# Performance work log

Measured on AMD Instinct MI355X. Metric: run time of the kernel, lower is better.

The kernel has to match this reference:

```python
import jax, jax.numpy as jnp
import numpy as np

B = 16384          # batch_size
NF = 50            # n_fields
K = 16             # embedding_dim
V = 1_000_000      # input_dim (vocab)
H = 400            # fc hidden
NNZ = B * NF


def _xavier(key, shape):
    fan_in, fan_out = shape
    lim = (6.0 / (fan_in + fan_out)) ** 0.5
    return jax.random.uniform(key, shape, minval=-lim, maxval=lim, dtype=jnp.float32)


def setup_inputs() -> dict:
    key = jax.random.key(0)
    ks = jax.random.split(key, 12)
    feats = jax.random.randint(ks[0], (NNZ,), 0, V)
    # n_fields contiguous features per sample (required by view(batch_size,-1))
    index = jnp.repeat(jnp.arange(B), NF)
    values = jax.random.uniform(ks[1], (NNZ,), dtype=jnp.float32)
    bias = jnp.zeros((1, 1), jnp.float32)
    weights = _xavier(ks[2], (V, 1))
    embedding = _xavier(ks[3], (V, K))
    d = NF * K  # 800
    W0 = _xavier(ks[4], (d, H))
    b0 = jax.random.normal(ks[5], (1, 1), jnp.float32)
    W1 = _xavier(ks[6], (H, H))
    b1 = jax.random.normal(ks[7], (1, 1), jnp.float32)
    W2 = _xavier(ks[8], (H, 1))
    b2 = jax.random.normal(ks[9], (1, 1), jnp.float32)
    return dict(index=index, feats=feats, values=values, bias=bias,
                weights=weights, embedding=embedding,
                W0=W0, b0=b0, W1=W1, b1=b1, W2=W2, b2=b2, batch_size=B)


def reference(index, feats, values, bias, weights, embedding,
              W0, b0, W1, b1, W2, b2, batch_size):
    # gather (F.embedding)
    w = weights[feats, 0]              # [nnz]
    emb = embedding[feats]             # [nnz, K]

    # first order: segment-sum of w*v, plus bias ([B] + [1,1] -> [1,B], as in torch)
    first = jax.ops.segment_sum(w * values, index, num_segments=batch_size) + bias

    # second order: FM pooling trick, fused over all K dims in one segment reduce
    ev = emb * values[:, None]                                        # [nnz, K]
    s1 = jax.ops.segment_sum(ev, index, num_segments=batch_size)      # [B, K]
    s2 = jax.ops.segment_sum(ev * ev, index, num_segments=batch_size) # [B, K]
    second = 0.5 * jnp.sum(s1 * s1 - s2, axis=1)                      # [B]

    # higher order MLP (relu on every layer, scalar biases)
    x = emb.reshape(batch_size, -1)    # [B, NF*K]
    x = jax.nn.relu(x @ W0 + b0)
    x = jax.nn.relu(x @ W1 + b1)
    x = jax.nn.relu(x @ W2 + b2)       # [B, 1]
    higher = x.reshape(-1)             # [B]

    return jax.nn.sigmoid(first + second + higher)  # [1, B]
```

## Files before the change

### kernel.cpp

```cpp
#include <hip/hip_runtime.h>
#include <hip/hip_bf16.h>


#define BATCH 16384
#define NFLD  50
#define EK    16
#define DDIM  800
#define HDIM  400
#define HPAD  416
#define NPAD  512

#define TB_W0 400
#define TB_W1 208
#define TBLK  (TB_W0 + TB_W1)
#define GBLK  (BATCH / 16)

#define MROWS 64
#define NCOLS 448
#define WCOLS 112
#define NFRAG 7
#define P1    (DDIM / 32)
#define P2    (HPAD / 32)
#define H0S   424
#define NCHUNK (NCOLS / 16)

typedef __attribute__((ext_vector_type(8))) __bf16 bf16x8;
typedef __attribute__((ext_vector_type(4))) float  f32x4;

typedef const __attribute__((address_space(1))) unsigned int* gas_u32p;
typedef __attribute__((address_space(3))) unsigned int*       las_u32p;

__device__ __forceinline__ void gld_lds16(const void* g, void* l) {
    __builtin_amdgcn_global_load_lds((gas_u32p)g, (las_u32p)l, 16, 0, 0);
}

__device__ __forceinline__ bf16x8 cvt8(const float4 a, const float4 b) {
    union { __hip_bfloat16 h[8]; bf16x8 v; } u;
    u.h[0] = __float2bfloat16(a.x); u.h[1] = __float2bfloat16(a.y);
    u.h[2] = __float2bfloat16(a.z); u.h[3] = __float2bfloat16(a.w);
    u.h[4] = __float2bfloat16(b.x); u.h[5] = __float2bfloat16(b.y);
    u.h[6] = __float2bfloat16(b.z); u.h[7] = __float2bfloat16(b.w);
    return u.v;
}

__global__ __launch_bounds__(256) void prep_kernel(
    const float* __restrict__ W0, const float* __restrict__ W1,
    __hip_bfloat16* __restrict__ W0t, __hip_bfloat16* __restrict__ W1t,
    const int* __restrict__ feats, const float* __restrict__ values,
    const float* __restrict__ biasp, const float* __restrict__ weights,
    const float* __restrict__ embedding, float* __restrict__ fs)
{
    const int bid = blockIdx.x;
    if (bid < TBLK) {
        const int which = bid >= TB_W0;
        const int i  = which ? bid - TB_W0 : bid;
        const int nx = which ? 13 : 25;
        const int bx = i % nx, by = i / nx;
        const float* src = which ? W1 : W0;
        __hip_bfloat16* dst = which ? W1t : W0t;
        const int srcK = which ? HDIM : DDIM;
        const int dstCols = which ? HPAD : DDIM;

        __shared__ float tile[32][33];
        const int tx = threadIdx.x & 31, ty = threadIdx.x >> 5;
        const int k0 = bx * 32, n0 = by * 32;
#pragma unroll
        for (int r = 0; r < 4; ++r) {
            int k = k0 + ty + r * 8;
            int n = n0 + tx;
            float v = (k < srcK && n < HDIM) ? src[(long)k * HDIM + n] : 0.f;
            tile[ty + r * 8][tx] = v;
        }
        __syncthreads();
#pragma unroll
        for (int r = 0; r < 4; ++r) {
            int n = n0 + ty + r * 8;
            int k = k0 + tx;
            if (k < dstCols)
                dst[(long)n * dstCols + k] = __float2bfloat16(tile[tx][ty + r * 8]);
        }
        return;
    }

    const int wave = threadIdx.x >> 6;
    const int lane = threadIdx.x & 63;
    const int r    = lane >> 2, c = lane & 3;
    const int sbase = (bid - TBLK) * 16 + wave * 4;

    int   f[4] = {0, 0, 0, 0};
    float v[4] = {0.f, 0.f, 0.f, 0.f};
    float wsum[4] = {0.f, 0.f, 0.f, 0.f};
#pragma unroll
    for (int q = 0; q < 4; ++q) {
        const long base = (long)(sbase + q) * NFLD;
        if (lane < NFLD) {
            f[q] = feats[base + lane];
            v[q] = values[base + lane];
            wsum[q] = weights[f[q]] * v[q];
        }
    }

    int   fj[4][4]; float vj[4][4];
#pragma unroll
    for (int q = 0; q < 4; ++q)
#pragma unroll
        for (int p = 0; p < 4; ++p) {
            const int j = p * 16 + r;
            if (p < 3 || r < 2) {
                fj[q][p] = __shfl(f[q], j);
                vj[q][p] = __shfl(v[q], j);
            }
        }
    float4 e[4][4];
#pragma unroll
    for (int q = 0; q < 4; ++q)
#pragma unroll
        for (int p = 0; p < 4; ++p)
            if (p < 3 || r < 2)
                e[q][p] = *(const float4*)(embedding + (long)fj[q][p] * EK + c * 4);

#pragma unroll
    for (int q = 0; q < 4; ++q) {
        const int s = sbase + q;
        f32x4 s1 = {0.f, 0.f, 0.f, 0.f}, s2 = {0.f, 0.f, 0.f, 0.f};
#pragma unroll
        for (int p = 0; p < 4; ++p) {
            const int j = p * 16 + r;
            if (p < 3 || r < 2) {
                f32x4 ef = {e[q][p].x, e[q][p].y, e[q][p].z, e[q][p].w};
                f32x4 ev = ef * vj[q][p];
                s1 += ev;
                s2 += ev * ev;
            }
        }
#pragma unroll
        for (int m = 4; m <= 32; m <<= 1) {
            s1.x += __shfl_xor(s1.x, m); s1.y += __shfl_xor(s1.y, m);
            s1.z += __shfl_xor(s1.z, m); s1.w += __shfl_xor(s1.w, m);
            s2.x += __shfl_xor(s2.x, m); s2.y += __shfl_xor(s2.y, m);
            s2.z += __shfl_xor(s2.z, m); s2.w += __shfl_xor(s2.w, m);
        }
        float t = (s1.x * s1.x - s2.x) + (s1.y * s1.y - s2.y)
                + (s1.z * s1.z - s2.z) + (s1.w * s1.w - s2.w);
        t += __shfl_xor(t, 1); t += __shfl_xor(t, 2);
        float w = wsum[q];
        w += __shfl_xor(w, 1);  w += __shfl_xor(w, 2);
        w += __shfl_xor(w, 4);  w += __shfl_xor(w, 8);
        w += __shfl_xor(w, 16); w += __shfl_xor(w, 32);
        if (lane == 0) fs[s] = w + 0.5f * t + biasp[0];
    }
}

__global__ __launch_bounds__(512, 2) void fused_mlp_kernel(
    const int* __restrict__ feats, const float* __restrict__ embedding,
    const __hip_bfloat16* __restrict__ W0t, const __hip_bfloat16* __restrict__ W1t,
    const float* __restrict__ b0p, const float* __restrict__ b1p,
    const float* __restrict__ W2, const float* __restrict__ b2p,
    const float* __restrict__ fs, float* __restrict__ out)
{
    __shared__ __align__(16) __hip_bfloat16 sB[2][NCOLS * 32];
    __shared__ __align__(16) __hip_bfloat16 h0p[MROWS * H0S];
    __shared__ int   sfeat[MROWS * NFLD];
    __shared__ float red[MROWS][4];

    const int tid  = threadIdx.x;
    const int wave = tid >> 6, lane = tid & 63;
    const int l16  = lane & 15, quad = lane >> 4;
    const int waveM = wave & 1, waveN = wave >> 1;
    const int m0 = blockIdx.x * MROWS;

    for (int i = tid; i < MROWS * NFLD; i += 512)
        sfeat[i] = feats[(long)m0 * NFLD + i];

    const float b0 = b0p[0];
    const float b1 = b1p[0];

    auto stageB = [&](const __hip_bfloat16* Bt, int ldb, int k0, int h) {
#pragma unroll
        for (int c = 0; c < 4; ++c) {
            const int ch = wave + c * 8;
            if (ch < NCHUNK) {
                const __hip_bfloat16* src =
                    Bt + (long)(ch * 16 + (lane >> 2)) * ldb + k0 + (lane & 3) * 8;
                gld_lds16(src, &sB[h][ch * 512 + lane * 8]);
            }
        }
    };

    auto loadA = [&](int p, float4* rg) {
        const int f  = p * 2 + (quad >> 1);
        const int d0 = (quad & 1) * 8;
#pragma unroll
        for (int i = 0; i < 2; ++i) {
            const int row = waveM * 32 + i * 16 + l16;
            const long fi = sfeat[row * NFLD + f];
            const float* ep = embedding + fi * EK + d0;
            rg[2 * i]     = *(const float4*)ep;
            rg[2 * i + 1] = *(const float4*)(ep + 4);
        }
    };

    f32x4 acc[2][NFRAG] = {};

    __syncthreads();
    float4 ra[4];
    loadA(0, ra);
    stageB(W0t, DDIM, 0, 0);
    __syncthreads();

#pragma unroll
    for (int p = 0; p < P1; ++p) {
        const int h = p & 1;
        float4 rn[4];
        if (p + 1 < P1) {
            stageB(W0t, DDIM, (p + 1) * 32, h ^ 1);
            loadA(p + 1, rn);
        }
        bf16x8 af[2];
        af[0] = cvt8(ra[0], ra[1]);
        af[1] = cvt8(ra[2], ra[3]);
        bf16x8 bfr[NFRAG];
#pragma unroll
        for (int j = 0; j < NFRAG; ++j)
            bfr[j] = *(const bf16x8*)&sB[h][(waveN * WCOLS + j * 16 + l16) * 32 + quad * 8];
#pragma unroll
        for (int i = 0; i < 2; ++i)
#pragma unroll
            for (int j = 0; j < NFRAG; ++j)
                acc[i][j] = __builtin_amdgcn_mfma_f32_16x16x32_bf16(
                    af[i], bfr[j], acc[i][j], 0, 0, 0);
        __syncthreads();
        if (p + 1 < P1) {
#pragma unroll
            for (int q = 0; q < 4; ++q) ra[q] = rn[q];
        }
    }

#pragma unroll
    for (int i = 0; i < 2; ++i)
#pragma unroll
        for (int j = 0; j < NFRAG; ++j) {
            const int col = waveN * WCOLS + j * 16 + l16;
            if (col < HPAD) {
#pragma unroll
                for (int r = 0; r < 4; ++r) {
                    const int row = waveM * 32 + i * 16 + quad * 4 + r;
                    float v = acc[i][j][r] + b0;
                    v = v > 0.f ? v : 0.f;
                    if (col >= HDIM) v = 0.f;
                    h0p[row * H0S + col] = __float2bfloat16(v);
                }
            }
        }

    f32x4 acc2[2][NFRAG] = {};
    stageB(W1t, HPAD, 0, 0);
    float w2v[NFRAG];
#pragma unroll
    for (int j = 0; j < NFRAG; ++j) {
        const int col = waveN * WCOLS + j * 16 + l16;
        w2v[j] = (col < HDIM) ? W2[col] : 0.f;
    }
    __syncthreads();

#pragma unroll
    for (int p = 0; p < P2; ++p) {
        const int h = p & 1;
        if (p + 1 < P2)
            stageB(W1t, HPAD, (p + 1) * 32, h ^ 1);
        bf16x8 af[2];
#pragma unroll
        for (int i = 0; i < 2; ++i)
            af[i] = *(const bf16x8*)&h0p[(waveM * 32 + i * 16 + l16) * H0S + p * 32 + quad * 8];
        bf16x8 bfr[NFRAG];
#pragma unroll
        for (int j = 0; j < NFRAG; ++j)
            bfr[j] = *(const bf16x8*)&sB[h][(waveN * WCOLS + j * 16 + l16) * 32 + quad * 8];
#pragma unroll
        for (int i = 0; i < 2; ++i)
#pragma unroll
            for (int j = 0; j < NFRAG; ++j)
                acc2[i][j] = __builtin_amdgcn_mfma_f32_16x16x32_bf16(
                    af[i], bfr[j], acc2[i][j], 0, 0, 0);
        __syncthreads();
    }

#pragma unroll
    for (int i = 0; i < 2; ++i)
#pragma unroll
        for (int r = 0; r < 4; ++r) {
            float ps = 0.f;
#pragma unroll
            for (int j = 0; j < NFRAG; ++j) {
                float v = acc2[i][j][r] + b1;
                v = v > 0.f ? v : 0.f;
                ps += v * w2v[j];
            }
            ps += __shfl_xor(ps, 1); ps += __shfl_xor(ps, 2);
            ps += __shfl_xor(ps, 4); ps += __shfl_xor(ps, 8);
            if (l16 == 0)
                red[waveM * 32 + i * 16 + quad * 4 + r][waveN] = ps;
        }
    __syncthreads();

    if (tid < MROWS) {
        const float s = (red[tid][0] + red[tid][1]) + (red[tid][2] + red[tid][3]);
        float hv = s + b2p[0];
        hv = hv > 0.f ? hv : 0.f;
        const float z = fs[m0 + tid] + hv;
        out[m0 + tid] = 1.f / (1.f + __expf(-z));
    }
}

extern "C" void kernel_launch(void* const* d_in, const int* in_sizes, int n_in,
                              void* d_out, int out_size, void* d_ws, size_t ws_size,
                              hipStream_t stream)
{
    const int*   feats     = (const int*)d_in[1];
    const float* values    = (const float*)d_in[2];
    const float* bias      = (const float*)d_in[3];
    const float* weights   = (const float*)d_in[4];
    const float* embedding = (const float*)d_in[5];
    const float* W0 = (const float*)d_in[6];
    const float* b0 = (const float*)d_in[7];
    const float* W1 = (const float*)d_in[8];
    const float* b1 = (const float*)d_in[9];
    const float* W2 = (const float*)d_in[10];
    const float* b2 = (const float*)d_in[11];

    char* ws = (char*)d_ws;
    size_t off = 0;
    auto alloc = [&](size_t bytes) {
        void* p = ws + off;
        off += (bytes + 255) & ~(size_t)255;
        return p;
    };
    float*          fs   = (float*)alloc((size_t)BATCH * 4);
    __hip_bfloat16* W0t  = (__hip_bfloat16*)alloc((size_t)NPAD * DDIM * 2);
    __hip_bfloat16* W1t  = (__hip_bfloat16*)alloc((size_t)NPAD * HPAD * 2);
    (void)ws_size; (void)in_sizes; (void)n_in; (void)out_size;

    prep_kernel<<<dim3(TBLK + GBLK), 256, 0, stream>>>(
        W0, W1, W0t, W1t, feats, values, bias, weights, embedding, fs);
    fused_mlp_kernel<<<dim3(BATCH / MROWS), 512, 0, stream>>>(
        feats, embedding, W0t, W1t, b0, b1, W2, b2, fs, (float*)d_out);
}
```

Before: 187.1 us.

## Materialize bf16 embedding matrix in prep kernel and stage A tiles via LDS DMA

The prep kernel, which already gathers the embeddings for the FM terms, now also writes them as a bf16 [B,800] matrix in workspace. The MLP kernel then loads A tiles with global_load_lds DMA alongside the W0 tiles, instead of doing a dependent feature lookup, float gather and register-side bf16 conversion per step. The K loops are also restructured to stage two k-tiles and then compute both between barriers, rather than using a prefetch-next pipeline. This removes the scattered gather latency from the GEMM loop, at the cost of writing and re-reading about 26 MB of intermediate data and losing compute/load overlap inside the loop.

```diff
diff --git a/kernel.cpp b/kernel.cpp
--- a/kernel.cpp
+++ b/kernel.cpp
@@ -34,21 +34,13 @@
     __builtin_amdgcn_global_load_lds((gas_u32p)g, (las_u32p)l, 16, 0, 0);
 }
 
-__device__ __forceinline__ bf16x8 cvt8(const float4 a, const float4 b) {
-    union { __hip_bfloat16 h[8]; bf16x8 v; } u;
-    u.h[0] = __float2bfloat16(a.x); u.h[1] = __float2bfloat16(a.y);
-    u.h[2] = __float2bfloat16(a.z); u.h[3] = __float2bfloat16(a.w);
-    u.h[4] = __float2bfloat16(b.x); u.h[5] = __float2bfloat16(b.y);
-    u.h[6] = __float2bfloat16(b.z); u.h[7] = __float2bfloat16(b.w);
-    return u.v;
-}
-
 __global__ __launch_bounds__(256) void prep_kernel(
     const float* __restrict__ W0, const float* __restrict__ W1,
     __hip_bfloat16* __restrict__ W0t, __hip_bfloat16* __restrict__ W1t,
     const int* __restrict__ feats, const float* __restrict__ values,
     const float* __restrict__ biasp, const float* __restrict__ weights,
-    const float* __restrict__ embedding, float* __restrict__ fs)
+    const float* __restrict__ embedding,
+    float* __restrict__ fs, __hip_bfloat16* __restrict__ x)
 {
     const int bid = blockIdx.x;
     if (bid < TBLK) {
@@ -131,6 +123,10 @@
                 f32x4 ev = ef * vj[q][p];
                 s1 += ev;
                 s2 += ev * ev;
+                __hip_bfloat16 pk[4] = {
+                    __float2bfloat16(e[q][p].x), __float2bfloat16(e[q][p].y),
+                    __float2bfloat16(e[q][p].z), __float2bfloat16(e[q][p].w)};
+                *(uint2*)&x[(long)s * DDIM + j * EK + c * 4] = *(uint2*)pk;
             }
         }
 #pragma unroll
@@ -152,15 +148,15 @@
 }
 
 __global__ __launch_bounds__(512, 2) void fused_mlp_kernel(
-    const int* __restrict__ feats, const float* __restrict__ embedding,
+    const __hip_bfloat16* __restrict__ x,
     const __hip_bfloat16* __restrict__ W0t, const __hip_bfloat16* __restrict__ W1t,
     const float* __restrict__ b0p, const float* __restrict__ b1p,
     const float* __restrict__ W2, const float* __restrict__ b2p,
     const float* __restrict__ fs, float* __restrict__ out)
 {
+    __shared__ __align__(16) __hip_bfloat16 sA[2][MROWS * 32];
     __shared__ __align__(16) __hip_bfloat16 sB[2][NCOLS * 32];
     __shared__ __align__(16) __hip_bfloat16 h0p[MROWS * H0S];
-    __shared__ int   sfeat[MROWS * NFLD];
     __shared__ float red[MROWS][4];
 
     const int tid  = threadIdx.x;
@@ -168,58 +164,44 @@
     const int l16  = lane & 15, quad = lane >> 4;
     const int waveM = wave & 1, waveN = wave >> 1;
     const int m0 = blockIdx.x * MROWS;
-
-    for (int i = tid; i < MROWS * NFLD; i += 512)
-        sfeat[i] = feats[(long)m0 * NFLD + i];
+    const int rlane = lane >> 2, clane = (lane & 3) * 8;
 
     const float b0 = b0p[0];
     const float b1 = b1p[0];
 
-    auto stageB = [&](const __hip_bfloat16* Bt, int ldb, int k0, int h) {
+    auto stage1 = [&](int p, int h) {
+        const int k0 = p * 32;
+#pragma unroll
+        for (int c = 0; c < 4; ++c) {
+            const int idx = wave * 4 + c;
+            if (idx < 4) {
+                gld_lds16(x + (long)(m0 + idx * 16 + rlane) * DDIM + k0 + clane,
+                          &sA[h][idx * 512 + lane * 8]);
+            } else {
+                const int ch = idx - 4;
+                gld_lds16(W0t + (long)(ch * 16 + rlane) * DDIM + k0 + clane,
+                          &sB[h][ch * 512 + lane * 8]);
+            }
+        }
+    };
+    auto stage2 = [&](int p, int h) {
+        const int k0 = p * 32;
 #pragma unroll
         for (int c = 0; c < 4; ++c) {
             const int ch = wave + c * 8;
             if (ch < NCHUNK) {
-                const __hip_bfloat16* src =
-                    Bt + (long)(ch * 16 + (lane >> 2)) * ldb + k0 + (lane & 3) * 8;
-                gld_lds16(src, &sB[h][ch * 512 + lane * 8]);
-            }
-        }
-    };
-
-    auto loadA = [&](int p, float4* rg) {
-        const int f  = p * 2 + (quad >> 1);
-        const int d0 = (quad & 1) * 8;
-#pragma unroll
-        for (int i = 0; i < 2; ++i) {
-            const int row = waveM * 32 + i * 16 + l16;
-            const long fi = sfeat[row * NFLD + f];
-            const float* ep = embedding + fi * EK + d0;
-            rg[2 * i]     = *(const float4*)ep;
-            rg[2 * i + 1] = *(const float4*)(ep + 4);
+                gld_lds16(W1t + (long)(ch * 16 + rlane) * HPAD + k0 + clane,
+                          &sB[h][ch * 512 + lane * 8]);
+            }
         }
     };
 
     f32x4 acc[2][NFRAG] = {};
-
-    __syncthreads();
-    float4 ra[4];
-    loadA(0, ra);
-    stageB(W0t, DDIM, 0, 0);
-    __syncthreads();
-
-#pragma unroll
-    for (int p = 0; p < P1; ++p) {
-        const int h = p & 1;
-        float4 rn[4];
-        if (p + 1 < P1) {
-            stageB(W0t, DDIM, (p + 1) * 32, h ^ 1);
-            loadA(p + 1, rn);
-        }
-        bf16x8 af[2];
-        af[0] = cvt8(ra[0], ra[1]);
-        af[1] = cvt8(ra[2], ra[3]);
-        bf16x8 bfr[NFRAG];
+    auto compute1 = [&](int h) {
+        bf16x8 af[2], bfr[NFRAG];
+#pragma unroll
+        for (int i = 0; i < 2; ++i)
+            af[i] = *(const bf16x8*)&sA[h][(waveM * 32 + i * 16 + l16) * 32 + quad * 8];
 #pragma unroll
         for (int j = 0; j < NFRAG; ++j)
             bfr[j] = *(const bf16x8*)&sB[h][(waveN * WCOLS + j * 16 + l16) * 32 + quad * 8];
@@ -229,12 +211,18 @@
             for (int j = 0; j < NFRAG; ++j)
                 acc[i][j] = __builtin_amdgcn_mfma_f32_16x16x32_bf16(
                     af[i], bfr[j], acc[i][j], 0, 0, 0);
-        __syncthreads();
-        if (p + 1 < P1) {
-#pragma unroll
-            for (int q = 0; q < 4; ++q) ra[q] = rn[q];
-        }
-    }
+    };
+
+    for (int kt = 0; kt + 1 < P1; kt += 2) {
+        stage1(kt, 0); stage1(kt + 1, 1);
+        __syncthreads();
+        compute1(0); compute1(1);
+        __syncthreads();
+    }
+    stage1(P1 - 1, 0);
+    __syncthreads();
+    compute1(0);
+    __syncthreads();
 
 #pragma unroll
     for (int i = 0; i < 2; ++i)
@@ -254,25 +242,17 @@
         }
 
     f32x4 acc2[2][NFRAG] = {};
-    stageB(W1t, HPAD, 0, 0);
     float w2v[NFRAG];
 #pragma unroll
     for (int j = 0; j < NFRAG; ++j) {
         const int col = waveN * WCOLS + j * 16 + l16;
         w2v[j] = (col < HDIM) ? W2[col] : 0.f;
     }
-    __syncthreads();
-
-#pragma unroll
-    for (int p = 0; p < P2; ++p) {
-        const int h = p & 1;
-        if (p + 1 < P2)
-            stageB(W1t, HPAD, (p + 1) * 32, h ^ 1);
-        bf16x8 af[2];
+    auto compute2 = [&](int h, int p) {
+        bf16x8 af[2], bfr[NFRAG];
 #pragma unroll
         for (int i = 0; i < 2; ++i)
             af[i] = *(const bf16x8*)&h0p[(waveM * 32 + i * 16 + l16) * H0S + p * 32 + quad * 8];
-        bf16x8 bfr[NFRAG];
 #pragma unroll
         for (int j = 0; j < NFRAG; ++j)
             bfr[j] = *(const bf16x8*)&sB[h][(waveN * WCOLS + j * 16 + l16) * 32 + quad * 8];
@@ -282,8 +262,17 @@
             for (int j = 0; j < NFRAG; ++j)
                 acc2[i][j] = __builtin_amdgcn_mfma_f32_16x16x32_bf16(
                     af[i], bfr[j], acc2[i][j], 0, 0, 0);
-        __syncthreads();
-    }
+    };
+
+    for (int kt = 0; kt + 1 < P2; kt += 2) {
+        stage2(kt, 0); stage2(kt + 1, 1);
+        __syncthreads();
+        compute2(0, kt); compute2(1, kt + 1);
+        __syncthreads();
+    }
+    stage2(P2 - 1, 0);
+    __syncthreads();
+    compute2(0, P2 - 1);
 
 #pragma unroll
     for (int i = 0; i < 2; ++i)
@@ -336,12 +325,13 @@
         return p;
     };
     float*          fs   = (float*)alloc((size_t)BATCH * 4);
+    __hip_bfloat16* x    = (__hip_bfloat16*)alloc((size_t)BATCH * DDIM * 2);
     __hip_bfloat16* W0t  = (__hip_bfloat16*)alloc((size_t)NPAD * DDIM * 2);
     __hip_bfloat16* W1t  = (__hip_bfloat16*)alloc((size_t)NPAD * HPAD * 2);
     (void)ws_size; (void)in_sizes; (void)n_in; (void)out_size;
 
     prep_kernel<<<dim3(TBLK + GBLK), 256, 0, stream>>>(
-        W0, W1, W0t, W1t, feats, values, bias, weights, embedding, fs);
+        W0, W1, W0t, W1t, feats, values, bias, weights, embedding, fs, x);
     fused_mlp_kernel<<<dim3(BATCH / MROWS), 512, 0, stream>>>(
-        feats, embedding, W0t, W1t, b0, b1, W2, b2, fs, (float*)d_out);
+        x, W0t, W1t, b0, b1, W2, b2, fs, (float*)d_out);
 }
```

Result: faster. 181.1 us (-3.2%).
